# Performance work log

Measured on AMD Instinct MI355X. Metric: run time of the kernel, lower is better.

The kernel has to match this reference:

```python
import jax, jax.numpy as jnp
import numpy as np

B, N, D, H = 4, 4096, 1024, 16
HD = D // H  # 64
EPS_NORM = 1e-12  # F.normalize eps
EPS_LN = 1e-5     # layernorm eps


def setup_inputs() -> dict:
    key = jax.random.key(0)
    ks = jax.random.split(key, 9)
    s = 0.02
    return {
        "x": jax.random.normal(ks[0], (B, N, D), jnp.float32),
        "Wq": jax.random.normal(ks[1], (D, D), jnp.float32) * s,
        "Wk": jax.random.normal(ks[2], (D, D), jnp.float32) * s,
        "Wv": jax.random.normal(ks[3], (D, D), jnp.float32) * s,
        "Wf": jax.random.normal(ks[4], (H, D), jnp.float32) * s,
        "Wg1": jax.random.normal(ks[5], (HD, D), jnp.float32) * s,
        "Wg2": jax.random.normal(ks[6], (D, HD), jnp.float32) * s,
        "ln_w": jnp.ones((D,), jnp.float32),
        "Wo": jax.random.normal(ks[7], (D, D), jnp.float32) * s,
    }


def _silu(x):
    return x * jax.nn.sigmoid(x)


def _simple_gla(q, k, v, f):
    # q,k,v: [B,N,H,HD], f: [B,N,H] log-decay. Recurrence:
    #   S_t = exp(f_t) * S_{t-1} + k_t v_t^T ;  o_t = q_t^T S_t  (scale=1)
    qT = jnp.moveaxis(q, 1, 0)  # [N,B,H,HD]
    kT = jnp.moveaxis(k, 1, 0)
    vT = jnp.moveaxis(v, 1, 0)
    fT = jnp.moveaxis(f, 1, 0)  # [N,B,H]

    def step(S, inp):
        qt, kt, vt, ft = inp
        S = jnp.exp(ft)[..., None, None] * S + kt[..., :, None] * vt[..., None, :]
        o = jnp.einsum('bhk,bhkv->bhv', qt, S)
        return S, o

    S0 = jnp.zeros((q.shape[0], q.shape[2], q.shape[3], v.shape[3]), q.dtype)
    _, o = jax.lax.scan(step, S0, (qT, kT, vT, fT))
    return jnp.moveaxis(o, 0, 1)  # [B,N,H,HD]


def reference(x, Wq, Wk, Wv, Wf, Wg1, Wg2, ln_w, Wo):
    b, n, d = x.shape
    q = _silu(x @ Wq.T).reshape(b, n, H, HD)
    k = _silu(x @ Wk.T).reshape(b, n, H, HD)
    v = _silu(x @ Wv.T).reshape(b, n, H, HD)
    f = jax.nn.log_sigmoid(x @ Wf.T)  # [B,N,H] scalar per-head log decay
    # F.normalize(k, p=2, dim=-1)
    k = k / jnp.maximum(jnp.linalg.norm(k, axis=-1, keepdims=True), EPS_NORM)

    o = _simple_gla(q, k, v, f).reshape(b, n, d)

    # output gate: sigmoid(Linear(d->hd) -> Linear(hd->d))
    gate = jax.nn.sigmoid((x @ Wg1.T) @ Wg2.T)
    o = o * gate

    # layernorm without bias
    mu = jnp.mean(o, axis=-1, keepdims=True)
    xc = o - mu
    var = jnp.mean(xc * xc, axis=-1, keepdims=True)
    o = xc / jnp.sqrt(var + EPS_LN) * ln_w

    return o @ Wo.T
```

## Files before the change

kernel.cpp:

```cpp
#include <hip/hip_runtime.h>
#include <stdint.h>


#define NWIDE 3200

typedef __attribute__((ext_vector_type(4))) float f32x4;
typedef __attribute__((ext_vector_type(4))) unsigned short u16x4;
typedef __attribute__((ext_vector_type(8))) unsigned short u16x8;
typedef __attribute__((ext_vector_type(8))) __bf16 bf16x8;

__device__ __forceinline__ float bf2f(unsigned short u) {
    union { unsigned int i; float f; } c; c.i = ((unsigned int)u) << 16; return c.f;
}
__device__ __forceinline__ unsigned short f2bf(float f) {
    union { float f; unsigned int i; } c; c.f = f;
    return (unsigned short)((c.i + 0x7fffu + ((c.i >> 16) & 1u)) >> 16);
}
__device__ __forceinline__ float siluf(float x) { return x / (1.f + __expf(-x)); }
__device__ __forceinline__ float logsigf(float z) {
    return (z >= 0.f) ? -log1pf(__expf(-z)) : (z - log1pf(__expf(z)));
}
__device__ __forceinline__ f32x4 MFMA(bf16x8 a, bf16x8 b, f32x4 c) {
    return __builtin_amdgcn_mfma_f32_16x16x32_bf16(a, b, c, 0, 0, 0);
}
__device__ __forceinline__ void lds16(const void* g, void* l) {
    __builtin_amdgcn_global_load_lds(
        (const __attribute__((address_space(1))) unsigned int*)(uintptr_t)g,
        (__attribute__((address_space(3))) unsigned int*)(unsigned int)(uintptr_t)l,
        16, 0, 0);
}

__global__ __launch_bounds__(256)
void k_prep(const float* __restrict__ x, const float* __restrict__ Wq, const float* __restrict__ Wk,
            const float* __restrict__ Wv, const float* __restrict__ Wf, const float* __restrict__ Wg1,
            const float* __restrict__ Wg2, const float* __restrict__ lnw, const float* __restrict__ Wo,
            unsigned short* __restrict__ xb, unsigned short* __restrict__ Wcat,
            unsigned short* __restrict__ Wob, unsigned short* __restrict__ Wg2b,
            float* __restrict__ scol) {
    const int blk = blockIdx.x, t = threadIdx.x;
    if (blk < 16384) {
        const int i = blk * 256 + t;
        f32x4 v = ((const f32x4*)x)[i];
        u16x4 o;
#pragma unroll
        for (int e = 0; e < 4; e++) o[e] = f2bf(v[e]);
        ((u16x4*)xb)[i] = o;
    } else if (blk < 19584) {
        const int r = blk - 16384;
        const float* src = nullptr; int sr = r;
        if (r < 1024) { src = Wq; }
        else if (r < 2048) { src = Wk; sr = r - 1024; }
        else if (r < 3072) { src = Wv; sr = r - 2048; }
        else if (r < 3088) { src = Wf; sr = r - 3072; }
        else if (r < 3152) { src = Wg1; sr = r - 3088; }
        u16x4 o;
        if (src) {
            f32x4 v = *(const f32x4*)&src[(size_t)sr * 1024 + 4 * t];
#pragma unroll
            for (int e = 0; e < 4; e++) o[e] = f2bf(v[e]);
        } else {
            o[0] = 0; o[1] = 0; o[2] = 0; o[3] = 0;
        }
        *(u16x4*)&Wcat[(size_t)r * 1024 + 4 * t] = o;
    } else if (blk < 20608) {
        __shared__ float red[4];
        const int c = blk - 19584;
        f32x4 wv = *(const f32x4*)&Wo[(size_t)c * 1024 + 4 * t];
        f32x4 lv = *(const f32x4*)&lnw[4 * t];
        u16x4 o; float ps = 0.f;
#pragma unroll
        for (int e = 0; e < 4; e++) { o[e] = f2bf(wv[e] * lv[e]); ps += bf2f(o[e]); }
        *(u16x4*)&Wob[(size_t)c * 1024 + 4 * t] = o;
#pragma unroll
        for (int m = 1; m < 64; m <<= 1) ps += __shfl_xor(ps, m, 64);
        if ((t & 63) == 0) red[t >> 6] = ps;
        __syncthreads();
        if (t == 0) scol[c] = red[0] + red[1] + red[2] + red[3];
    } else {
        const int i = (blk - 20608) * 256 + t;
        f32x4 v = ((const f32x4*)Wg2)[i];
        u16x4 o;
#pragma unroll
        for (int e = 0; e < 4; e++) o[e] = f2bf(v[e]);
        ((u16x4*)Wg2b)[i] = o;
    }
}

template <int MODE>
__global__ __launch_bounds__(256)
void k_gemm(const unsigned short* __restrict__ A, const unsigned short* __restrict__ Bw,
            void* __restrict__ outp, float* __restrict__ zbuf,
            const float* __restrict__ stats, const float* __restrict__ scol,
            int M, int N, int K, int ldOut) {
    __shared__ __align__(16) unsigned short As[128 * 64];
    __shared__ __align__(16) unsigned short Bs[128 * 64];
    const int tid = threadIdx.x;
    const int w = tid >> 6, lane = tid & 63;
    const int m0 = blockIdx.x * 128, n0 = blockIdx.y * 128;
    const int fr = lane & 15, fg = lane >> 4;
    const int wr = w >> 1, wc = w & 1;
    const int srow = lane >> 3;
    const int schunk = (lane & 7) ^ (srow & 7);
    f32x4 acc[4][4] = {};
    const int kc = K >> 6;
    for (int kt = 0; kt < kc; ++kt) {
        const int k0 = kt << 6;
        __syncthreads();
#pragma unroll
        for (int q = 0; q < 4; q++) {
            const int rr = 32 * w + 8 * q;
            lds16(A + (size_t)(m0 + rr + srow) * K + k0 + schunk * 8, &As[rr * 64]);
            lds16(Bw + (size_t)(n0 + rr + srow) * K + k0 + schunk * 8, &Bs[rr * 64]);
        }
        __syncthreads();
        bf16x8 av[4][2], bv[4][2];
#pragma unroll
        for (int i = 0; i < 4; i++)
#pragma unroll
            for (int ks = 0; ks < 2; ks++) {
                const int row = 64 * wr + 16 * i + fr;
                av[i][ks] = *(const bf16x8*)&As[row * 64 + (((ks * 4 + fg) ^ (row & 7)) << 3)];
            }
#pragma unroll
        for (int j = 0; j < 4; j++)
#pragma unroll
            for (int ks = 0; ks < 2; ks++) {
                const int row = 64 * wc + 16 * j + fr;
                bv[j][ks] = *(const bf16x8*)&Bs[row * 64 + (((ks * 4 + fg) ^ (row & 7)) << 3)];
            }
#pragma unroll
        for (int i = 0; i < 4; i++)
#pragma unroll
            for (int j = 0; j < 4; j++)
#pragma unroll
                for (int ks = 0; ks < 2; ks++)
                    acc[i][j] = MFMA(av[i][ks], bv[j][ks], acc[i][j]);
    }
    const int nb = n0 + 64 * wc;
    if (MODE == 1) {
        float* O = (float*)outp;
        float sj[4];
#pragma unroll
        for (int j = 0; j < 4; j++) sj[j] = scol[nb + 16 * j + fr];
#pragma unroll
        for (int i = 0; i < 4; i++)
#pragma unroll
            for (int r = 0; r < 4; r++) {
                const int gr = m0 + 64 * wr + 16 * i + 4 * fg + r;
                const float mu = stats[gr * 2], rs = stats[gr * 2 + 1];
#pragma unroll
                for (int j = 0; j < 4; j++)
                    O[(size_t)gr * ldOut + nb + 16 * j + fr] = rs * (acc[i][j][r] - mu * sj[j]);
            }
        return;
    }
    unsigned short* Y = (unsigned short*)outp;
    if (nb >= 3072) {
#pragma unroll
        for (int i = 0; i < 4; i++)
#pragma unroll
            for (int j = 0; j < 4; j++) {
                const int gc = nb + 16 * j + fr;
#pragma unroll
                for (int r = 0; r < 4; r++) {
                    const int gr = m0 + 64 * wr + 16 * i + 4 * fg + r;
                    const float v = acc[i][j][r];
                    if (gc < 3088) {
                        if (gc >= 3072) zbuf[gr * 16 + (gc - 3072)] = v;
                    } else if (gc < 3152) {
                        Y[(size_t)gr * ldOut + gc] = f2bf(v);
                    }
                }
            }
    } else {
#pragma unroll
        for (int i = 0; i < 4; i++)
#pragma unroll
            for (int j = 0; j < 4; j++) {
                const int gc = nb + 16 * j + fr;
#pragma unroll
                for (int r = 0; r < 4; r++)
                    Y[(size_t)(m0 + 64 * wr + 16 * i + 4 * fg + r) * ldOut + gc] = f2bf(acc[i][j][r]);
            }
    }
}

__global__ __launch_bounds__(256)
void k_chunk_kv(const unsigned short* __restrict__ Y, const float* __restrict__ zbuf,
                float* __restrict__ cbuf, unsigned short* __restrict__ St) {
    __shared__ __align__(16) unsigned short Kt[64 * 72];
    __shared__ __align__(16) unsigned short Vt[64 * 72];
    __shared__ float cs[64];
    const int cid = blockIdx.x, tid = threadIdx.x;
    const int bh = cid >> 6, ic = cid & 63;
    const int b = bh >> 4, h = bh & 15;
    if (tid < 64) {
        float v = logsigf(zbuf[(size_t)(b * 4096 + ic * 64 + tid) * 16 + h]);
#pragma unroll
        for (int off = 1; off < 64; off <<= 1) {
            float u = __shfl_up(v, (unsigned)off, 64);
            if (tid >= off) v += u;
        }
        cs[tid] = v;
        cbuf[(size_t)cid * 64 + tid] = v;
    }
    __syncthreads();
    const int s = tid >> 2, c0 = (tid & 3) << 4;
    const float wdec = __expf(cs[63] - cs[s]);
    const size_t rowg = (size_t)(b * 4096 + ic * 64 + s) * NWIDE;
    u16x8 k0v = *(const u16x8*)&Y[rowg + 1024 + h * 64 + c0];
    u16x8 k1v = *(const u16x8*)&Y[rowg + 1024 + h * 64 + c0 + 8];
    u16x8 v0v = *(const u16x8*)&Y[rowg + 2048 + h * 64 + c0];
    u16x8 v1v = *(const u16x8*)&Y[rowg + 2048 + h * 64 + c0 + 8];
    float kf[16]; float ss = 0.f;
#pragma unroll
    for (int e = 0; e < 8; e++) { kf[e] = siluf(bf2f(k0v[e])); ss += kf[e] * kf[e]; }
#pragma unroll
    for (int e = 0; e < 8; e++) { kf[8 + e] = siluf(bf2f(k1v[e])); ss += kf[8 + e] * kf[8 + e]; }
    ss += __shfl_xor(ss, 1, 64);
    ss += __shfl_xor(ss, 2, 64);
    const float sc = wdec / fmaxf(sqrtf(ss), 1e-12f);
#pragma unroll
    for (int e = 0; e < 8; e++) {
        Kt[(c0 + e) * 72 + s] = f2bf(kf[e] * sc);
        Kt[(c0 + 8 + e) * 72 + s] = f2bf(kf[8 + e] * sc);
        Vt[(c0 + e) * 72 + s] = f2bf(siluf(bf2f(v0v[e])));
        Vt[(c0 + 8 + e) * 72 + s] = f2bf(siluf(bf2f(v1v[e])));
    }
    __syncthreads();
    const int w = tid >> 6, lane = tid & 63;
    const int fr = lane & 15, fg = lane >> 4;
    f32x4 acc[4] = {};
#pragma unroll
    for (int ks = 0; ks < 2; ks++) {
        bf16x8 a = *(const bf16x8*)&Kt[(16 * w + fr) * 72 + ks * 32 + fg * 8];
#pragma unroll
        for (int j = 0; j < 4; j++)
            acc[j] = MFMA(a, *(const bf16x8*)&Vt[(16 * j + fr) * 72 + ks * 32 + fg * 8], acc[j]);
    }
    unsigned short* outp = St + (size_t)cid * 4096;
#pragma unroll
    for (int j = 0; j < 4; j++)
#pragma unroll
        for (int r = 0; r < 4; r++)
            outp[(16 * w + 4 * fg + r) * 64 + 16 * j + fr] = f2bf(acc[j][r]);
}

__global__ __launch_bounds__(256)
void k_scan(unsigned short* __restrict__ St, const float* __restrict__ cbuf) {
    const int bh = blockIdx.x >> 2;
    const int e0 = (((blockIdx.x & 3) << 8) + threadIdx.x) << 2;
    float S[4] = {0.f, 0.f, 0.f, 0.f};
    const size_t base = (size_t)bh * 64 * 4096 + e0;
    for (int i = 0; i < 64; i++) {
        const float d = __expf(cbuf[(bh * 64 + i) * 64 + 63]);
        u16x4 m = *(u16x4*)&St[base + (size_t)i * 4096];
        u16x4 o;
#pragma unroll
        for (int e = 0; e < 4; e++) { o[e] = f2bf(S[e]); S[e] = d * S[e] + bf2f(m[e]); }
        *(u16x4*)&St[base + (size_t)i * 4096] = o;
    }
}

__global__ __launch_bounds__(256)
void k_chunk_out(const unsigned short* __restrict__ Y, const float* __restrict__ cbuf,
                 const unsigned short* __restrict__ St, const unsigned short* __restrict__ Wg2b,
                 unsigned short* __restrict__ og) {
    __shared__ __align__(16) unsigned short Qs[64 * 72];
    __shared__ __align__(16) unsigned short Ks[64 * 72];
    __shared__ __align__(16) unsigned short Vt[64 * 72];
    __shared__ __align__(16) unsigned short S0[64 * 72];
    __shared__ __align__(16) unsigned short G1[64 * 72];
    __shared__ __align__(16) unsigned short W2[64 * 72];
    __shared__ __align__(16) unsigned short Pl[4 * 16 * 72];
    __shared__ float cs[64];
    const int cid = blockIdx.x, tid = threadIdx.x;
    const int bh = cid >> 6, ic = cid & 63;
    const int b = bh >> 4, h = bh & 15;
    if (tid < 64) cs[tid] = cbuf[(size_t)cid * 64 + tid];
    const int s = tid >> 2, c0 = (tid & 3) << 4;
    const size_t rowg = (size_t)(b * 4096 + ic * 64 + s) * NWIDE;
    {
        u16x8 q0 = *(const u16x8*)&Y[rowg + h * 64 + c0];
        u16x8 q1 = *(const u16x8*)&Y[rowg + h * 64 + c0 + 8];
        u16x8 o0, o1;
#pragma unroll
        for (int e = 0; e < 8; e++) { o0[e] = f2bf(siluf(bf2f(q0[e]))); o1[e] = f2bf(siluf(bf2f(q1[e]))); }
        *(u16x8*)&Qs[s * 72 + c0] = o0;
        *(u16x8*)&Qs[s * 72 + c0 + 8] = o1;
    }
    {
        u16x8 k0v = *(const u16x8*)&Y[rowg + 1024 + h * 64 + c0];
        u16x8 k1v = *(const u16x8*)&Y[rowg + 1024 + h * 64 + c0 + 8];
        float kf[16]; float ssn = 0.f;
#pragma unroll
        for (int e = 0; e < 8; e++) { kf[e] = siluf(bf2f(k0v[e])); ssn += kf[e] * kf[e]; }
#pragma unroll
        for (int e = 0; e < 8; e++) { kf[8 + e] = siluf(bf2f(k1v[e])); ssn += kf[8 + e] * kf[8 + e]; }
        ssn += __shfl_xor(ssn, 1, 64);
        ssn += __shfl_xor(ssn, 2, 64);
        const float scn = 1.f / fmaxf(sqrtf(ssn), 1e-12f);
        u16x8 o0, o1;
#pragma unroll
        for (int e = 0; e < 8; e++) { o0[e] = f2bf(kf[e] * scn); o1[e] = f2bf(kf[8 + e] * scn); }
        *(u16x8*)&Ks[s * 72 + c0] = o0;
        *(u16x8*)&Ks[s * 72 + c0 + 8] = o1;
    }
    *(u16x8*)&G1[s * 72 + c0] = *(const u16x8*)&Y[rowg + 3088 + c0];
    *(u16x8*)&G1[s * 72 + c0 + 8] = *(const u16x8*)&Y[rowg + 3088 + c0 + 8];
    *(u16x8*)&W2[s * 72 + c0] = *(const u16x8*)&Wg2b[(size_t)(h * 64 + s) * 64 + c0];
    *(u16x8*)&W2[s * 72 + c0 + 8] = *(const u16x8*)&Wg2b[(size_t)(h * 64 + s) * 64 + c0 + 8];
    {
        u16x8 v0v = *(const u16x8*)&Y[rowg + 2048 + h * 64 + c0];
        u16x8 v1v = *(const u16x8*)&Y[rowg + 2048 + h * 64 + c0 + 8];
        u16x8 s0v = *(const u16x8*)&St[(size_t)cid * 4096 + s * 64 + c0];
        u16x8 s1v = *(const u16x8*)&St[(size_t)cid * 4096 + s * 64 + c0 + 8];
#pragma unroll
        for (int e = 0; e < 8; e++) {
            Vt[(c0 + e) * 72 + s] = f2bf(siluf(bf2f(v0v[e])));
            Vt[(c0 + 8 + e) * 72 + s] = f2bf(siluf(bf2f(v1v[e])));
            S0[(c0 + e) * 72 + s] = s0v[e];
            S0[(c0 + 8 + e) * 72 + s] = s1v[e];
        }
    }
    __syncthreads();
    const int w = tid >> 6, lane = tid & 63;
    const int fr = lane & 15, fg = lane >> 4;
    bf16x8 aq[2];
#pragma unroll
    for (int ks = 0; ks < 2; ks++) aq[ks] = *(const bf16x8*)&Qs[(16 * w + fr) * 72 + ks * 32 + fg * 8];
    f32x4 sc[4] = {};
#pragma unroll
    for (int ks = 0; ks < 2; ks++)
#pragma unroll
        for (int j = 0; j < 4; j++)
            sc[j] = MFMA(aq[ks], *(const bf16x8*)&Ks[(16 * j + fr) * 72 + ks * 32 + fg * 8], sc[j]);
    const int tl = 16 * w + 4 * fg;
#pragma unroll
    for (int j = 0; j < 4; j++)
#pragma unroll
        for (int r = 0; r < 4; r++) {
            const int tt = tl + r, ss2 = 16 * j + fr;
            float p = (ss2 <= tt) ? sc[j][r] * __expf(cs[tt] - cs[ss2]) : 0.f;
            Pl[w * (16 * 72) + (4 * fg + r) * 72 + ss2] = f2bf(p);
        }
    __syncthreads();
    f32x4 ov[4] = {};
#pragma unroll
    for (int ks = 0; ks < 2; ks++) {
        bf16x8 ap = *(const bf16x8*)&Pl[w * (16 * 72) + fr * 72 + ks * 32 + fg * 8];
#pragma unroll
        for (int j = 0; j < 4; j++)
            ov[j] = MFMA(ap, *(const bf16x8*)&Vt[(16 * j + fr) * 72 + ks * 32 + fg * 8], ov[j]);
    }
    f32x4 qs[4] = {};
#pragma unroll
    for (int ks = 0; ks < 2; ks++)
#pragma unroll
        for (int j = 0; j < 4; j++)
            qs[j] = MFMA(aq[ks], *(const bf16x8*)&S0[(16 * j + fr) * 72 + ks * 32 + fg * 8], qs[j]);
    bf16x8 ag[2];
#pragma unroll
    for (int ks = 0; ks < 2; ks++) ag[ks] = *(const bf16x8*)&G1[(16 * w + fr) * 72 + ks * 32 + fg * 8];
    f32x4 gl[4] = {};
#pragma unroll
    for (int ks = 0; ks < 2; ks++)
#pragma unroll
        for (int j = 0; j < 4; j++)
            gl[j] = MFMA(ag[ks], *(const bf16x8*)&W2[(16 * j + fr) * 72 + ks * 32 + fg * 8], gl[j]);
#pragma unroll
    for (int j = 0; j < 4; j++)
#pragma unroll
        for (int r = 0; r < 4; r++) {
            const int tt = tl + r;
            const float o = ov[j][r] + __expf(cs[tt]) * qs[j][r];
            const float g = 1.f / (1.f + __expf(-gl[j][r]));
            og[(size_t)(b * 4096 + ic * 64 + tt) * 1024 + h * 64 + 16 * j + fr] = f2bf(o * g);
        }
}

__global__ __launch_bounds__(256)
void k_lnstats(const unsigned short* __restrict__ og, float* __restrict__ stats) {
    const int row = blockIdx.x * 4 + (threadIdx.x >> 6);
    const int lane = threadIdx.x & 63;
    const unsigned short* p = og + (size_t)row * 1024 + lane * 16;
    u16x8 a = *(const u16x8*)p;
    u16x8 b2 = *(const u16x8*)(p + 8);
    float s = 0.f, q = 0.f;
#pragma unroll
    for (int e = 0; e < 8; e++) { float x = bf2f(a[e]); s += x; q += x * x; }
#pragma unroll
    for (int e = 0; e < 8; e++) { float x = bf2f(b2[e]); s += x; q += x * x; }
#pragma unroll
    for (int m = 1; m < 64; m <<= 1) { s += __shfl_xor(s, m, 64); q += __shfl_xor(q, m, 64); }
    if (lane == 0) {
        const float mu = s * (1.f / 1024.f);
        const float var = q * (1.f / 1024.f) - mu * mu;
        stats[row * 2] = mu;
        stats[row * 2 + 1] = rsqrtf(var + 1e-5f);
    }
}

extern "C" void kernel_launch(void* const* d_in, const int* in_sizes, int n_in,
                              void* d_out, int out_size, void* d_ws, size_t ws_size,
                              hipStream_t stream) {
    const float* x = (const float*)d_in[0];
    const float* Wq = (const float*)d_in[1];
    const float* Wk = (const float*)d_in[2];
    const float* Wv = (const float*)d_in[3];
    const float* Wf = (const float*)d_in[4];
    const float* Wg1 = (const float*)d_in[5];
    const float* Wg2 = (const float*)d_in[6];
    const float* lnw = (const float*)d_in[7];
    const float* Wo = (const float*)d_in[8];
    char* ws = (char*)d_ws;
    unsigned short* xb = (unsigned short*)(ws + 0);
    unsigned short* Yb = (unsigned short*)(ws + 33554432LL);
    unsigned short* Wcat = (unsigned short*)(ws + 138412032LL);
    unsigned short* Wob = (unsigned short*)(ws + 144965632LL);
    unsigned short* Wg2b = (unsigned short*)(ws + 147062784LL);
    float* zbuf = (float*)(ws + 147193856LL);
    float* cbuf = (float*)(ws + 148242432LL);
    unsigned short* St = (unsigned short*)(ws + 149291008LL);
    float* scol = (float*)(ws + 182845440LL);
    float* stats = (float*)(ws + 182849536LL);
    unsigned short* og = xb;

    k_prep<<<20672, 256, 0, stream>>>(x, Wq, Wk, Wv, Wf, Wg1, Wg2, lnw, Wo,
                                      xb, Wcat, Wob, Wg2b, scol);
    k_gemm<0><<<dim3(128, 25), 256, 0, stream>>>(xb, Wcat, Yb, zbuf, nullptr, nullptr,
                                                 16384, 3200, 1024, 3200);
    k_chunk_kv<<<4096, 256, 0, stream>>>(Yb, zbuf, cbuf, St);
    k_scan<<<256, 256, 0, stream>>>(St, cbuf);
    k_chunk_out<<<4096, 256, 0, stream>>>(Yb, cbuf, St, Wg2b, og);
    k_lnstats<<<4096, 256, 0, stream>>>(og, stats);
    k_gemm<1><<<dim3(128, 8), 256, 0, stream>>>(og, Wob, d_out, nullptr, stats, scol,
                                                16384, 1024, 1024, 1024);
}
```

Before: 332.3 us.

## Restructure output GEMM to keep full-K A rows in LDS, stream B from global

Splits the templated GEMM into two kernels and gives the final output projection its own kernel. The new kernel loads a 64x1024 slab of the normalized activations into LDS once per block (128 KB, swizzled), and 8 waves each cover 64 output columns in two passes, streaming weight fragments straight from global with register double-buffering. This removes per-K-tile barriers and the repeated A tile reloads of the old 128x128 tiled kernel. In exchange it uses a large LDS footprint that limits occupancy to one block per CU, and B is read from global or cache without LDS staging, with only 256 blocks in the grid.

```diff
diff --git a/kernel.cpp b/kernel.cpp
--- a/kernel.cpp
+++ b/kernel.cpp
@@ -86,12 +86,9 @@
     }
 }
 
-template <int MODE>
-__global__ __launch_bounds__(256)
-void k_gemm(const unsigned short* __restrict__ A, const unsigned short* __restrict__ Bw,
-            void* __restrict__ outp, float* __restrict__ zbuf,
-            const float* __restrict__ stats, const float* __restrict__ scol,
-            int M, int N, int K, int ldOut) {
+__global__ __launch_bounds__(256)
+void k_gemm1(const unsigned short* __restrict__ A, const unsigned short* __restrict__ Bw,
+             unsigned short* __restrict__ Y, float* __restrict__ zbuf, int K, int ldOut) {
     __shared__ __align__(16) unsigned short As[128 * 64];
     __shared__ __align__(16) unsigned short Bs[128 * 64];
     const int tid = threadIdx.x;
@@ -137,24 +134,6 @@
                     acc[i][j] = MFMA(av[i][ks], bv[j][ks], acc[i][j]);
     }
     const int nb = n0 + 64 * wc;
-    if (MODE == 1) {
-        float* O = (float*)outp;
-        float sj[4];
-#pragma unroll
-        for (int j = 0; j < 4; j++) sj[j] = scol[nb + 16 * j + fr];
-#pragma unroll
-        for (int i = 0; i < 4; i++)
-#pragma unroll
-            for (int r = 0; r < 4; r++) {
-                const int gr = m0 + 64 * wr + 16 * i + 4 * fg + r;
-                const float mu = stats[gr * 2], rs = stats[gr * 2 + 1];
-#pragma unroll
-                for (int j = 0; j < 4; j++)
-                    O[(size_t)gr * ldOut + nb + 16 * j + fr] = rs * (acc[i][j][r] - mu * sj[j]);
-            }
-        return;
-    }
-    unsigned short* Y = (unsigned short*)outp;
     if (nb >= 3072) {
 #pragma unroll
         for (int i = 0; i < 4; i++)
@@ -183,6 +162,78 @@
                     Y[(size_t)(m0 + 64 * wr + 16 * i + 4 * fg + r) * ldOut + gc] = f2bf(acc[i][j][r]);
             }
     }
+}
+
+__global__ __launch_bounds__(512)
+void k_gemm2(const unsigned short* __restrict__ Aog, const unsigned short* __restrict__ Bw,
+             float* __restrict__ O, const float* __restrict__ stats, const float* __restrict__ scol) {
+    __shared__ __align__(16) unsigned short As[64 * 1024];
+    const int tid = threadIdx.x;
+    const int w = tid >> 6, lane = tid & 63;
+    const int fr = lane & 15, fg = lane >> 4;
+    const int R0 = blockIdx.x * 64;
+#pragma unroll
+    for (int q = 0; q < 16; q++) {
+        const int cl = q * 512 + w * 64;
+        const int c_lin = cl + lane;
+        const int r = c_lin >> 7, c = c_lin & 127;
+        const int csrc = (c & ~7) | ((c & 7) ^ (r & 7));
+        lds16(Aog + (size_t)(R0 + r) * 1024 + csrc * 8, (char*)As + (size_t)cl * 16);
+    }
+    __syncthreads();
+    const int swz7 = fr & 7;
+    const char* abase[4];
+#pragma unroll
+    for (int i = 0; i < 4; i++) abase[i] = (const char*)As + (16 * i + fr) * 2048;
+
+#define LDA_(dst, kk)                                                         \
+    do {                                                                      \
+        _Pragma("unroll")                                                     \
+        for (int i_ = 0; i_ < 4; i_++)                                        \
+            dst[i_] = *(const bf16x8*)(abase[i_] + (((4 * (kk) + fg) ^ swz7) << 4)); \
+    } while (0)
+
+    for (int g = 0; g < 2; ++g) {
+        const int nb = g * 512 + w * 64;
+        const unsigned short* pB[4];
+#pragma unroll
+        for (int j = 0; j < 4; j++) pB[j] = Bw + (size_t)(nb + 16 * j + fr) * 1024 + fg * 8;
+        f32x4 acc[4][4] = {};
+        bf16x8 bA[4], bB[4], a[4];
+#pragma unroll
+        for (int j = 0; j < 4; j++) bA[j] = *(const bf16x8*)(pB[j]);
+#pragma unroll 2
+        for (int kk = 0; kk < 32; kk += 2) {
+#pragma unroll
+            for (int j = 0; j < 4; j++) bB[j] = *(const bf16x8*)(pB[j] + (kk + 1) * 32);
+            LDA_(a, kk);
+#pragma unroll
+            for (int i = 0; i < 4; i++)
+#pragma unroll
+                for (int j = 0; j < 4; j++) acc[i][j] = MFMA(a[i], bA[j], acc[i][j]);
+#pragma unroll
+            for (int j = 0; j < 4; j++) bA[j] = *(const bf16x8*)(pB[j] + (kk + 2) * 32);
+            LDA_(a, kk + 1);
+#pragma unroll
+            for (int i = 0; i < 4; i++)
+#pragma unroll
+                for (int j = 0; j < 4; j++) acc[i][j] = MFMA(a[i], bB[j], acc[i][j]);
+        }
+        float sj[4];
+#pragma unroll
+        for (int j = 0; j < 4; j++) sj[j] = scol[nb + 16 * j + fr];
+#pragma unroll
+        for (int i = 0; i < 4; i++)
+#pragma unroll
+            for (int r = 0; r < 4; r++) {
+                const int gr = R0 + 16 * i + 4 * fg + r;
+                const float mu = stats[gr * 2], rs = stats[gr * 2 + 1];
+#pragma unroll
+                for (int j = 0; j < 4; j++)
+                    O[(size_t)gr * 1024 + nb + 16 * j + fr] = rs * (acc[i][j][r] - mu * sj[j]);
+            }
+    }
+#undef LDA_
 }
 
 __global__ __launch_bounds__(256)
@@ -428,12 +479,10 @@
 
     k_prep<<<20672, 256, 0, stream>>>(x, Wq, Wk, Wv, Wf, Wg1, Wg2, lnw, Wo,
                                       xb, Wcat, Wob, Wg2b, scol);
-    k_gemm<0><<<dim3(128, 25), 256, 0, stream>>>(xb, Wcat, Yb, zbuf, nullptr, nullptr,
-                                                 16384, 3200, 1024, 3200);
+    k_gemm1<<<dim3(128, 25), 256, 0, stream>>>(xb, Wcat, Yb, zbuf, 1024, 3200);
     k_chunk_kv<<<4096, 256, 0, stream>>>(Yb, zbuf, cbuf, St);
     k_scan<<<256, 256, 0, stream>>>(St, cbuf);
     k_chunk_out<<<4096, 256, 0, stream>>>(Yb, cbuf, St, Wg2b, og);
     k_lnstats<<<4096, 256, 0, stream>>>(og, stats);
-    k_gemm<1><<<dim3(128, 8), 256, 0, stream>>>(og, Wob, d_out, nullptr, stats, scol,
-                                                16384, 1024, 1024, 1024);
-}
+    k_gemm2<<<256, 512, 0, stream>>>(og, Wob, (float*)d_out, stats, scol);
+}
```

After: 350.6 us. +5.5%, slower.
